# Optimization experiments

Measured on AMD Instinct MI355X. Metric: run time of the kernel, lower is better.

Reference implementation:

```python
import jax, jax.numpy as jnp
import numpy as np

B = 4
G = 1024                      # GridSize
H = 1.0 / (G - 1)             # h = (right-left)/(GridSize-1), area=[[0,0],[1,1]]
GD = 0.0                      # boundary value for hard_encode padding


def _cross(a):
    # sum of 4-neighborhood: matches conv2d with kernel [[0,.5,0],[.5,0,.5],[0,.5,0]] / 0.5
    return a[..., :-2, 1:-1] + a[..., 2:, 1:-1] + a[..., 1:-1, :-2] + a[..., 1:-1, 2:]


def _inner(a):
    return a[..., 1:-1, 1:-1]


def kappa(x, mu):
    # assumed parameterization (kappa undefined in source): exp(mu * x)
    return jnp.exp(mu * x)


def setup_inputs() -> dict:
    key = jax.random.key(0)
    k1, k2, k3, k4 = jax.random.split(key, 4)
    pre = jax.random.normal(k1, (B, 1, G - 2, G - 2), jnp.float32)
    f = jax.random.normal(k2, (B, 1, G, G), jnp.float32)
    mu = jax.random.uniform(k3, (1,), jnp.float32)
    prev_pre = jax.random.normal(k4, (B, 1, G, G), jnp.float32) * 0.1
    return {"pre": pre, "f": f, "mu": mu, "prev_pre": prev_pre, "maxiter": 20}


def reference(pre, f, mu, prev_pre, maxiter):
    # w = kappa(prev_pre, mu) is iteration-invariant -> hoist out of the loop
    w = kappa(prev_pre, mu)            # [B,1,G,G]
    w_in = _inner(w)                   # [B,1,G-2,G-2]
    force = _inner(f) * (H * H)
    # k3 conv: 0.5*cross + 2*center
    y3 = 0.5 * _cross(w) + 2.0 * w_in

    def step(y, _):
        u = jnp.pad(y, ((0, 0), (0, 0), (1, 1), (1, 1)), constant_values=GD)
        y1 = 0.5 * _cross(u) * w_in    # conv(u, k1) * w_inner
        y2 = 0.5 * _cross(w * u)       # conv(w*u, k2)
        return (force + y1 + y2) / y3, None

    # original: one jac_step, then `maxiter` more -> maxiter+1 total
    y, _ = jax.lax.scan(step, pre, None, length=maxiter + 1)
    return y
```

## Files before the change

kernel.cpp:

```cpp
#include <hip/hip_runtime.h>

#define BB 4
#define GG 1024
#define NI 1022
#define HH2 (2.0f / (1023.0f * 1023.0f))
#define TK 21
#define TB 128
#define OFF 24
#define TOUT 80
#define NT 13
#define HS 132

typedef float vf4 __attribute__((ext_vector_type(4)));
typedef float vf2 __attribute__((ext_vector_type(2)));

__global__ __launch_bounds__(1024)
void pinn_mega(const float* __restrict__ pre,
               const float* __restrict__ fglob,
               const float* __restrict__ mu_p,
               const float* __restrict__ pp,
               float* __restrict__ yout)
{
    __shared__ float wh[2 * 16 * HS];
    __shared__ float yh[2][2 * 16 * HS];

    const int tid = threadIdx.x;
    const int tx = tid & 31, ty = tid >> 5;
    const int lane = tid & 63;
    const int s = ty >> 1;
    const int odd = ty & 1;
    const int b  = blockIdx.z;
    const int AR = blockIdx.y * TOUT - OFF;
    const int A0 = blockIdx.x * TOUT - OFF;
    const int R  = 4 * ty;
    const int c0 = 4 * tx;
    const float mu = mu_p[0];

    const int cb = min(max(A0 + c0, 0), GG - 4);
    const size_t pb = (size_t)b * GG * GG;
    const int r0 = min(max(AR + R,     0), GG - 1);
    const int r1 = min(max(AR + R + 1, 0), GG - 1);
    const int r2 = min(max(AR + R + 2, 0), GG - 1);
    const int r3 = min(max(AR + R + 3, 0), GG - 1);
    const int r4 = min(max(AR + R + 4, 0), GG - 1);
    vf4 wv0 = *(const vf4*)&pp[pb + (size_t)r0 * GG + cb];
    vf4 wv1 = *(const vf4*)&pp[pb + (size_t)r1 * GG + cb];
    vf4 wv2 = *(const vf4*)&pp[pb + (size_t)r2 * GG + cb];
    vf4 wv3 = *(const vf4*)&pp[pb + (size_t)r3 * GG + cb];
    const vf4 fv0 = *(const vf4*)&fglob[pb + (size_t)r1 * GG + cb];
    const vf4 fv1 = *(const vf4*)&fglob[pb + (size_t)r2 * GG + cb];
    const vf4 fv2 = *(const vf4*)&fglob[pb + (size_t)r3 * GG + cb];
    const vf4 fv3 = *(const vf4*)&fglob[pb + (size_t)r4 * GG + cb];

    vf4 y0v, y1v, y2v, y3v;
    {
        const int i0 = min(max(AR + R,     0), NI - 1);
        const int i1 = min(max(AR + R + 1, 0), NI - 1);
        const int i2 = min(max(AR + R + 2, 0), NI - 1);
        const int i3 = min(max(AR + R + 3, 0), NI - 1);
        const int cy  = min(max(A0 + c0, 0), NI - 2);
        const int cy2 = min(cy + 2, NI - 2);
        #define LDY(dst, ii) { \
            const size_t base_ = (size_t)(b * NI + (ii)) * NI; \
            const vf2 a_ = *(const vf2*)&pre[base_ + cy]; \
            const vf2 b_ = *(const vf2*)&pre[base_ + cy2]; \
            dst[0] = a_[0]; dst[1] = a_[1]; dst[2] = b_[0]; dst[3] = b_[1]; }
        LDY(y0v, i0) LDY(y1v, i1) LDY(y2v, i2) LDY(y3v, i3)
        #undef LDY
    }

    #pragma unroll
    for (int m = 0; m < 4; ++m) {
        wv0[m] = __expf(mu * wv0[m]);
        wv1[m] = __expf(mu * wv1[m]);
        wv2[m] = __expf(mu * wv2[m]);
        wv3[m] = __expf(mu * wv3[m]);
    }
    if (!odd) {
        *(vf4*)&wh[s * HS + c0]        = wv0;
        *(vf4*)&wh[(16 + s) * HS + c0] = wv1;
    }
    __syncthreads();

    vf4 w4, w5;
    {
        const int so = min(s + 1, 15);
        const vf4 l4 = *(const vf4*)&wh[so * HS + c0];
        const vf4 l5 = *(const vf4*)&wh[(16 + so) * HS + c0];
        #pragma unroll
        for (int m = 0; m < 4; ++m) {
            const float x4 = __shfl_xor(wv0[m], 32, 64);
            const float x5 = __shfl_xor(wv1[m], 32, 64);
            w4[m] = odd ? l4[m] : x4;
            w5[m] = odd ? l5[m] : x5;
        }
    }

    const float s1_0 = __shfl(wv0[0], lane + 1, 64);
    const float s1_1 = __shfl(wv1[0], lane + 1, 64);
    const float s1_2 = __shfl(wv2[0], lane + 1, 64);
    const float s1_3 = __shfl(wv3[0], lane + 1, 64);
    const float s1_4 = __shfl(w4[0],  lane + 1, 64);
    const float s1_5 = __shfl(w5[0],  lane + 1, 64);
    const float s2_1 = __shfl(wv1[1], lane + 1, 64);
    const float s2_2 = __shfl(wv2[1], lane + 1, 64);
    const float s2_3 = __shfl(wv3[1], lane + 1, 64);
    const float s2_4 = __shfl(w4[1],  lane + 1, 64);
    const float sf0 = __shfl(fv0[0], lane + 1, 64);
    const float sf1 = __shfl(fv1[0], lane + 1, 64);
    const float sf2 = __shfl(fv2[0], lane + 1, 64);
    const float sf3 = __shfl(fv3[0], lane + 1, 64);

    vf4 bN0,bN1,bN2,bN3, bS0,bS1,bS2,bS3, bW0,bW1,bW2,bW3,
        bE0,bE1,bE2,bE3, bf0,bf1,bf2,bf3;

    #define COEFF(kk, N_, C_, S_, s1N, s1C, s1S, s2C, FV, SF, BN, BS, BW, BE, BF, YV) { \
        const vf4 wN = {N_[1], N_[2], N_[3], s1N}; \
        const vf4 wW = C_; \
        const vf4 wC = {C_[1], C_[2], C_[3], s1C}; \
        const vf4 wE = {C_[2], C_[3], s1C, s2C}; \
        const vf4 wS = {S_[1], S_[2], S_[3], s1S}; \
        const vf4 aN = wC + wN, aS = wC + wS, aW = wC + wW, aE = wC + wE; \
        const vf4 den = (aN + aS) + (aW + aE); \
        const int gi = AR + R + (kk); \
        vf4 rd; \
        _Pragma("unroll") \
        for (int m = 0; m < 4; ++m) { \
            float x = __builtin_amdgcn_rcpf(den[m]); \
            x = x * (2.0f - den[m] * x); \
            const int gj = A0 + c0 + m; \
            const bool in = (gi >= 0) && (gi < NI) && (gj >= 0) && (gj < NI); \
            rd[m] = in ? x : 0.0f; \
            YV[m] = in ? YV[m] : 0.0f; \
        } \
        BN = aN * rd; BS = aS * rd; BW = aW * rd; BE = aE * rd; \
        const vf4 fC = {FV[1], FV[2], FV[3], SF}; \
        BF = (fC * rd) * HH2; }

    COEFF(0, wv0, wv1, wv2, s1_0, s1_1, s1_2, s2_1, fv0, sf0, bN0,bS0,bW0,bE0,bf0, y0v)
    COEFF(1, wv1, wv2, wv3, s1_1, s1_2, s1_3, s2_2, fv1, sf1, bN1,bS1,bW1,bE1,bf1, y1v)
    COEFF(2, wv2, wv3, w4,  s1_2, s1_3, s1_4, s2_3, fv2, sf2, bN2,bS2,bW2,bE2,bf2, y2v)
    COEFF(3, wv3, w4,  w5,  s1_3, s1_4, s1_5, s2_4, fv3, sf3, bN3,bS3,bW3,bE3,bf3, y3v)
    #undef COEFF

    const int pubOff = (odd ? 16 * HS : 0) + s * HS + c0;
    const int halOff = odd ? (min(s + 1, 15) * HS + c0)
                           : ((16 + max(s - 1, 0)) * HS + c0);

    for (int t = 1; t <= TK; ++t) {
        float* buf = yh[t & 1];
        *(vf4*)&buf[pubOff] = odd ? y3v : y0v;
        __syncthreads();
        const vf4 hal = *(const vf4*)&buf[halOff];
        vf4 upx, dnx;
        #pragma unroll
        for (int m = 0; m < 4; ++m) {
            upx[m] = __shfl_xor(y3v[m], 32, 64);
            dnx[m] = __shfl_xor(y0v[m], 32, 64);
        }
        const vf4 up = odd ? upx : hal;
        const vf4 dn = odd ? hal : dnx;
        const float l0 = __shfl(y0v[3], lane - 1, 64), rr0 = __shfl(y0v[0], lane + 1, 64);
        const float l1 = __shfl(y1v[3], lane - 1, 64), rr1 = __shfl(y1v[0], lane + 1, 64);
        const float l2 = __shfl(y2v[3], lane - 1, 64), rr2 = __shfl(y2v[0], lane + 1, 64);
        const float l3 = __shfl(y3v[3], lane - 1, 64), rr3 = __shfl(y3v[0], lane + 1, 64);
        const vf4 yW0 = {l0, y0v[0], y0v[1], y0v[2]}, yE0 = {y0v[1], y0v[2], y0v[3], rr0};
        const vf4 yW1 = {l1, y1v[0], y1v[1], y1v[2]}, yE1 = {y1v[1], y1v[2], y1v[3], rr1};
        const vf4 yW2 = {l2, y2v[0], y2v[1], y2v[2]}, yE2 = {y2v[1], y2v[2], y2v[3], rr2};
        const vf4 yW3 = {l3, y3v[0], y3v[1], y3v[2]}, yE3 = {y3v[1], y3v[2], y3v[3], rr3};
        vf4 n0 = bf0; n0 += bN0 * up;  n0 += bS0 * y1v; n0 += bW0 * yW0; n0 += bE0 * yE0;
        vf4 n1 = bf1; n1 += bN1 * y0v; n1 += bS1 * y2v; n1 += bW1 * yW1; n1 += bE1 * yE1;
        vf4 n2 = bf2; n2 += bN2 * y1v; n2 += bS2 * y3v; n2 += bW2 * yW2; n2 += bE2 * yE2;
        vf4 n3 = bf3; n3 += bN3 * y2v; n3 += bS3 * dn;  n3 += bW3 * yW3; n3 += bE3 * yE3;
        y0v = n0; y1v = n1; y2v = n2; y3v = n3;
    }

    if (R >= OFF && R < OFF + TOUT && c0 >= OFF && c0 < OFF + TOUT) {
        const int gj0 = A0 + c0;
        #define STORE(kk, YV) { \
            const int gi = AR + R + (kk); \
            if (gi < NI) { \
                const size_t rb = (size_t)(b * NI + gi) * NI; \
                if (gj0 + 3 < NI) { \
                    vf2 pa, pv; pa[0]=YV[0]; pa[1]=YV[1]; pv[0]=YV[2]; pv[1]=YV[3]; \
                    *(vf2*)&yout[rb + gj0] = pa; *(vf2*)&yout[rb + gj0 + 2] = pv; \
                } else { \
                    _Pragma("unroll") \
                    for (int m = 0; m < 4; ++m) \
                        if (gj0 + m < NI) yout[rb + gj0 + m] = YV[m]; \
                } \
            } }
        STORE(0, y0v) STORE(1, y1v) STORE(2, y2v) STORE(3, y3v)
        #undef STORE
    }
}

extern "C" void kernel_launch(void* const* d_in, const int* in_sizes, int n_in,
                              void* d_out, int out_size, void* d_ws, size_t ws_size,
                              hipStream_t stream) {
    const float* pre = (const float*)d_in[0];
    const float* f   = (const float*)d_in[1];
    const float* mu  = (const float*)d_in[2];
    const float* pp  = (const float*)d_in[3];
    (void)d_ws; (void)ws_size;

    pinn_mega<<<dim3(NT, NT, BB), dim3(1024, 1, 1), 0, stream>>>(
        pre, f, mu, pp, (float*)d_out);
}
```

Measured before the change: 172.1 us.

## Split temporal-blocked Jacobi into two launches with smaller halo overlap

```diff
diff --git a/kernel.cpp b/kernel.cpp
--- a/kernel.cpp
+++ b/kernel.cpp
@@ -3,19 +3,20 @@
 #define BB 4
 #define GG 1024
 #define NI 1022
+#define SROW 1024
 #define HH2 (2.0f / (1023.0f * 1023.0f))
-#define TK 21
 #define TB 128
-#define OFF 24
-#define TOUT 80
-#define NT 13
+#define OFF 12
+#define TOUT 104
+#define NT 10
 #define HS 132
 
 typedef float vf4 __attribute__((ext_vector_type(4)));
 typedef float vf2 __attribute__((ext_vector_type(2)));
 
+template<int TKP, bool VIN4, bool VOUT4>
 __global__ __launch_bounds__(1024)
-void pinn_mega(const float* __restrict__ pre,
+void pinn_mega(const float* __restrict__ ysrc,
                const float* __restrict__ fglob,
                const float* __restrict__ mu_p,
                const float* __restrict__ pp,
@@ -58,15 +59,23 @@
         const int i1 = min(max(AR + R + 1, 0), NI - 1);
         const int i2 = min(max(AR + R + 2, 0), NI - 1);
         const int i3 = min(max(AR + R + 3, 0), NI - 1);
-        const int cy  = min(max(A0 + c0, 0), NI - 2);
-        const int cy2 = min(cy + 2, NI - 2);
-        #define LDY(dst, ii) { \
-            const size_t base_ = (size_t)(b * NI + (ii)) * NI; \
-            const vf2 a_ = *(const vf2*)&pre[base_ + cy]; \
-            const vf2 b_ = *(const vf2*)&pre[base_ + cy2]; \
-            dst[0] = a_[0]; dst[1] = a_[1]; dst[2] = b_[0]; dst[3] = b_[1]; }
-        LDY(y0v, i0) LDY(y1v, i1) LDY(y2v, i2) LDY(y3v, i3)
-        #undef LDY
+        if (VIN4) {
+            const int cy = min(max(A0 + c0, 0), SROW - 4);
+            y0v = *(const vf4*)&ysrc[(size_t)(b * NI + i0) * SROW + cy];
+            y1v = *(const vf4*)&ysrc[(size_t)(b * NI + i1) * SROW + cy];
+            y2v = *(const vf4*)&ysrc[(size_t)(b * NI + i2) * SROW + cy];
+            y3v = *(const vf4*)&ysrc[(size_t)(b * NI + i3) * SROW + cy];
+        } else {
+            const int cy  = min(max(A0 + c0, 0), NI - 2);
+            const int cy2 = min(cy + 2, NI - 2);
+            #define LDY(dst, ii) { \
+                const size_t base_ = (size_t)(b * NI + (ii)) * NI; \
+                const vf2 a_ = *(const vf2*)&ysrc[base_ + cy]; \
+                const vf2 b_ = *(const vf2*)&ysrc[base_ + cy2]; \
+                dst[0] = a_[0]; dst[1] = a_[1]; dst[2] = b_[0]; dst[3] = b_[1]; }
+            LDY(y0v, i0) LDY(y1v, i1) LDY(y2v, i2) LDY(y3v, i3)
+            #undef LDY
+        }
     }
 
     #pragma unroll
@@ -147,7 +156,7 @@
     const int halOff = odd ? (min(s + 1, 15) * HS + c0)
                            : ((16 + max(s - 1, 0)) * HS + c0);
 
-    for (int t = 1; t <= TK; ++t) {
+    for (int t = 1; t <= TKP; ++t) {
         float* buf = yh[t & 1];
         *(vf4*)&buf[pubOff] = odd ? y3v : y0v;
         __syncthreads();
@@ -177,21 +186,30 @@
 
     if (R >= OFF && R < OFF + TOUT && c0 >= OFF && c0 < OFF + TOUT) {
         const int gj0 = A0 + c0;
-        #define STORE(kk, YV) { \
-            const int gi = AR + R + (kk); \
-            if (gi < NI) { \
-                const size_t rb = (size_t)(b * NI + gi) * NI; \
-                if (gj0 + 3 < NI) { \
-                    vf2 pa, pv; pa[0]=YV[0]; pa[1]=YV[1]; pv[0]=YV[2]; pv[1]=YV[3]; \
-                    *(vf2*)&yout[rb + gj0] = pa; *(vf2*)&yout[rb + gj0 + 2] = pv; \
-                } else { \
-                    _Pragma("unroll") \
-                    for (int m = 0; m < 4; ++m) \
-                        if (gj0 + m < NI) yout[rb + gj0 + m] = YV[m]; \
-                } \
-            } }
-        STORE(0, y0v) STORE(1, y1v) STORE(2, y2v) STORE(3, y3v)
-        #undef STORE
+        if (VOUT4) {
+            #define STORE4(kk, YV) { \
+                const int gi = AR + R + (kk); \
+                if (gi < NI && gj0 + 3 < SROW) \
+                    *(vf4*)&yout[(size_t)(b * NI + gi) * SROW + gj0] = YV; }
+            STORE4(0, y0v) STORE4(1, y1v) STORE4(2, y2v) STORE4(3, y3v)
+            #undef STORE4
+        } else {
+            #define STORE(kk, YV) { \
+                const int gi = AR + R + (kk); \
+                if (gi < NI) { \
+                    const size_t rb = (size_t)(b * NI + gi) * NI; \
+                    if (gj0 + 3 < NI) { \
+                        vf2 pa, pv; pa[0]=YV[0]; pa[1]=YV[1]; pv[0]=YV[2]; pv[1]=YV[3]; \
+                        *(vf2*)&yout[rb + gj0] = pa; *(vf2*)&yout[rb + gj0 + 2] = pv; \
+                    } else { \
+                        _Pragma("unroll") \
+                        for (int m = 0; m < 4; ++m) \
+                            if (gj0 + m < NI) yout[rb + gj0 + m] = YV[m]; \
+                    } \
+                } }
+            STORE(0, y0v) STORE(1, y1v) STORE(2, y2v) STORE(3, y3v)
+            #undef STORE
+        }
     }
 }
 
@@ -202,8 +220,11 @@
     const float* f   = (const float*)d_in[1];
     const float* mu  = (const float*)d_in[2];
     const float* pp  = (const float*)d_in[3];
-    (void)d_ws; (void)ws_size;
-
-    pinn_mega<<<dim3(NT, NT, BB), dim3(1024, 1, 1), 0, stream>>>(
-        pre, f, mu, pp, (float*)d_out);
+
+    float* yA = (float*)d_ws;
+
+    const dim3 grid(NT, NT, BB);
+    const dim3 bs(1024, 1, 1);
+    pinn_mega<11, false, true ><<<grid, bs, 0, stream>>>(pre, f, mu, pp, yA);
+    pinn_mega<10, true,  false><<<grid, bs, 0, stream>>>(yA,  f, mu, pp, (float*)d_out);
 }
```

Result: slower. 185.4 us (+7.7%).
